# Kernel tuning notes

Measured on AMD Instinct MI355X. Metric: run time of the kernel, lower is better.

The kernel has to match this reference:

```python
import jax, jax.numpy as jnp
import numpy as np

NUM_CLASSES = 512  # P distinct identities in the batch (labels are in [0, P))
TAU = 0.5
EPS = 1e-12


def _l2norm(x):
    # F.normalize(x, dim=1) with eps clamp
    n = jnp.sqrt(jnp.sum(x * x, axis=1, keepdims=True))
    return x / jnp.maximum(n, EPS)


def setup_inputs() -> dict:
    key = jax.random.key(0)
    k1, k2, k3 = jax.random.split(key, 3)
    N, D, P = 8192, 2048, NUM_CLASSES
    feat_vp = jax.random.normal(k1, (N, D), dtype=jnp.float32)
    feat_ap = jax.random.normal(k2, (N, D), dtype=jnp.float32)
    feat_rp = jax.random.normal(k3, (N, D), dtype=jnp.float32)
    # P identities, K = N/P instances each; every class present
    label = (jnp.arange(N) % P).astype(jnp.int32)
    return {"feat_vp": feat_vp, "feat_ap": feat_ap, "feat_rp": feat_rp, "label": label}


def reference(feat_vp, feat_ap, feat_rp, label):
    P = NUM_CLASSES
    fv = _l2norm(feat_vp)
    fa = _l2norm(feat_ap)
    fr = _l2norm(feat_rp)

    # segment-mean over labels (replaces the O(N^2 D) python loop)
    counts = jax.ops.segment_sum(jnp.ones_like(label, dtype=fv.dtype), label,
                                 num_segments=P)  # [P]
    inv_cnt = 1.0 / counts[:, None]

    def centers(f):
        s = jax.ops.segment_sum(f, label, num_segments=P)  # [P, D]
        return _l2norm(s * inv_cnt)

    cv, ca, cr = centers(fv), centers(fa), centers(fr)

    # per-sample centers = unique centers gathered back by label
    loss_intra = (jnp.sum((fv - cv[label]) ** 2, axis=1).mean()
                  + jnp.sum((fa - ca[label]) ** 2, axis=1).mean()
                  + jnp.sum((fr - cr[label]) ** 2, axis=1).mean())

    def pair_loss(c1, c2):
        logits = (c1 @ c2.T) / TAU  # [P, P]
        logp = jax.nn.log_softmax(logits, axis=1)
        return -jnp.mean(jnp.diagonal(logp))

    loss_inter = pair_loss(cv, ca) + pair_loss(cv, cr) + pair_loss(ca, cr)
    return loss_intra + loss_inter
```

## Files before the change

### kernel.cpp

```cpp
#include <hip/hip_runtime.h>
#include <hip/hip_bf16.h>

#define P_CLS 512
#define D_DIM 2048
#define CAP   32
#define TAU_INV 2.0f

typedef short short8 __attribute__((ext_vector_type(8)));
typedef float f32x4 __attribute__((ext_vector_type(4)));

__device__ __forceinline__ unsigned short f2bf_bits(float x) {
  __hip_bfloat16 b = __float2bfloat16(x);
  unsigned short u;
  __builtin_memcpy(&u, &b, sizeof(u));
  return u;
}

__device__ __forceinline__ float xred_sum(float v) {
#pragma unroll
  for (int o = 1; o < 64; o <<= 1) v += __shfl_xor(v, o, 64);
  return v;
}
__device__ __forceinline__ float xred_max(float v) {
#pragma unroll
  for (int o = 1; o < 64; o <<= 1) v = fmaxf(v, __shfl_xor(v, o, 64));
  return v;
}

__global__ void k_init(int* cnt, float* accs) {
  int t = blockIdx.x * blockDim.x + threadIdx.x;
  if (t < P_CLS) cnt[t] = 0;
  if (t < 8) accs[t] = 0.f;
}

__global__ void k_index(const int* __restrict__ label, int* __restrict__ cnt,
                        int* __restrict__ idx, int n) {
  int i = blockIdx.x * blockDim.x + threadIdx.x;
  if (i < n) {
    int p = label[i];
    int slot = atomicAdd(&cnt[p], 1);
    if (slot < CAP) idx[p * CAP + slot] = i;
  }
}

__global__ __launch_bounds__(256)
void k_centers(const float* __restrict__ f0, const float* __restrict__ f1,
               const float* __restrict__ f2, const int* __restrict__ cnt,
               const int* __restrict__ idx, __hip_bfloat16* __restrict__ cb,
               float* __restrict__ accs) {
  __shared__ __align__(16) f32x4 red[4][D_DIM / 4];
  __shared__ float scr[4];
  int p = blockIdx.x, m = blockIdx.y;
  const float* F = (m == 0) ? f0 : (m == 1) ? f1 : f2;
  int t = threadIdx.x, lane = t & 63, wv = t >> 6;
  int c = cnt[p];
  if (c > CAP) c = CAP;
  const int* idxp = idx + p * CAP;

  int nr = (c > wv) ? ((c - wv + 3) >> 2) : 0;

  f32x4 acc[8] = {{0,0,0,0},{0,0,0,0},{0,0,0,0},{0,0,0,0},
                  {0,0,0,0},{0,0,0,0},{0,0,0,0},{0,0,0,0}};
  f32x4 a[8], b[8];

  auto loadrow = [&](f32x4* buf, int r) {
    const f32x4* rp = (const f32x4*)(F + (long)idxp[r] * D_DIM);
#pragma unroll
    for (int j = 0; j < 8; ++j) buf[j] = rp[lane + 64 * j];
  };
  auto consume = [&](const f32x4* buf) {
    float ssq = 0.f;
#pragma unroll
    for (int j = 0; j < 8; ++j) {
      f32x4 q = buf[j] * buf[j];
      ssq += q.x + q.y + q.z + q.w;
    }
    ssq = xred_sum(ssq);
    float w = 1.0f / fmaxf(sqrtf(ssq), 1e-12f);
#pragma unroll
    for (int j = 0; j < 8; ++j) acc[j] += buf[j] * w;
  };

  if (nr > 0) loadrow(a, wv);
  if (nr > 1) loadrow(b, wv + 4);
  for (int k = 0; k < nr; k += 2) {
    consume(a);
    if (k + 2 < nr) loadrow(a, wv + 4 * (k + 2));
    if (k + 1 < nr) {
      consume(b);
      if (k + 3 < nr) loadrow(b, wv + 4 * (k + 3));
    }
  }

#pragma unroll
  for (int j = 0; j < 8; ++j) red[wv][lane + 64 * j] = acc[j];
  __syncthreads();
  f32x4 s0 = red[0][t] + red[1][t] + red[2][t] + red[3][t];
  f32x4 s1 = red[0][t + 256] + red[1][t + 256] + red[2][t + 256] + red[3][t + 256];
  f32x4 q0 = s0 * s0, q1 = s1 * s1;
  float s2 = q0.x + q0.y + q0.z + q0.w + q1.x + q1.y + q1.z + q1.w;
  s2 = xred_sum(s2);
  if (lane == 0) scr[wv] = s2;
  __syncthreads();
  s2 = scr[0] + scr[1] + scr[2] + scr[3];
  float sn = sqrtf(s2);
  float inv = 1.0f / fmaxf(sn, 1e-12f);
  __hip_bfloat16* dst = cb + ((long)m * P_CLS + p) * D_DIM;
  f32x4 o0 = s0 * inv, o1 = s1 * inv;
  ushort4 h0, h1;
  h0.x = f2bf_bits(o0.x); h0.y = f2bf_bits(o0.y);
  h0.z = f2bf_bits(o0.z); h0.w = f2bf_bits(o0.w);
  h1.x = f2bf_bits(o1.x); h1.y = f2bf_bits(o1.y);
  h1.z = f2bf_bits(o1.z); h1.w = f2bf_bits(o1.w);
  ((ushort4*)dst)[t] = h0;
  ((ushort4*)dst)[t + 256] = h1;
  if (t == 0 && c > 0) atomicAdd(&accs[0], sn);
}

__global__ __launch_bounds__(256)
void k_gemm(const __hip_bfloat16* __restrict__ cbh, float* __restrict__ logits) {
  __shared__ __align__(16) unsigned short As[2][64 * 40], Bs[2][64 * 40];
  int pair = blockIdx.y, kz = blockIdx.z, nkz = gridDim.z;
  int ksl = D_DIM / nkz;
  int ma = (pair == 2) ? 1 : 0;
  int mb = (pair == 0) ? 1 : 2;
  const unsigned short* A =
      (const unsigned short*)cbh + (long)ma * P_CLS * D_DIM + kz * ksl;
  const unsigned short* B =
      (const unsigned short*)cbh + (long)mb * P_CLS * D_DIM + kz * ksl;
  float* C = logits + ((long)kz * 3 + pair) * P_CLS * P_CLS;
  int tm = (blockIdx.x >> 3) * 64, tn = (blockIdx.x & 7) * 64;
  int t = threadIdx.x, lane = t & 63, wv = t >> 6;
  int srow = t >> 2, skc = (t & 3) * 8;
  int quad = lane >> 4, mr = lane & 15;
  const unsigned short* pa = A + (long)(tm + srow) * D_DIM + skc;
  const unsigned short* pb = B + (long)(tn + srow) * D_DIM + skc;
  f32x4 acc[4] = {{0,0,0,0},{0,0,0,0},{0,0,0,0},{0,0,0,0}};
  uint4 av = *(const uint4*)pa, bv = *(const uint4*)pb;
  *(uint4*)(&As[0][srow * 40 + skc]) = av;
  *(uint4*)(&Bs[0][srow * 40 + skc]) = bv;
  av = *(const uint4*)(pa + 32); bv = *(const uint4*)(pb + 32);
  const int NIT = ksl / 32;
  for (int it = 0; it < NIT; ++it) {
    __syncthreads();
    int cur = it & 1;
    if (it + 1 < NIT) {
      *(uint4*)(&As[cur ^ 1][srow * 40 + skc]) = av;
      *(uint4*)(&Bs[cur ^ 1][srow * 40 + skc]) = bv;
    }
    if (it + 2 < NIT) {
      av = *(const uint4*)(pa + (it + 2) * 32);
      bv = *(const uint4*)(pb + (it + 2) * 32);
    }
    short8 af = *(const short8*)(&As[cur][(wv * 16 + mr) * 40 + quad * 8]);
#pragma unroll
    for (int nb = 0; nb < 4; ++nb) {
      short8 bfr = *(const short8*)(&Bs[cur][(nb * 16 + mr) * 40 + quad * 8]);
      acc[nb] = __builtin_amdgcn_mfma_f32_16x16x32_bf16(af, bfr, acc[nb], 0, 0, 0);
    }
  }
  int crow = tm + wv * 16 + quad * 4;
#pragma unroll
  for (int nb = 0; nb < 4; ++nb)
#pragma unroll
    for (int r = 0; r < 4; ++r)
      C[(long)(crow + r) * P_CLS + tn + nb * 16 + mr] = acc[nb][r] * TAU_INV;
}

__global__ __launch_bounds__(256)
void k_lse(const float* __restrict__ logits, float* __restrict__ accs, int nkz) {
  __shared__ float sred[8];
  int row = blockIdx.x;
  int p = row & (P_CLS - 1);
  int t = threadIdx.x, lane = t & 63, wv = t >> 6;
  float v0 = 0.f, v1 = 0.f, diag = 0.f;
  for (int z = 0; z < nkz; ++z) {
    const float* L = logits + ((long)z * 3 * P_CLS + row) * P_CLS;
    v0 += L[t];
    v1 += L[t + 256];
  }
  float mx = xred_max(fmaxf(v0, v1));
  if (lane == 0) sred[wv] = mx;
  __syncthreads();
  mx = fmaxf(fmaxf(sred[0], sred[1]), fmaxf(sred[2], sred[3]));
  float e = expf(v0 - mx) + expf(v1 - mx);
  e = xred_sum(e);
  if (lane == 0) sred[4 + wv] = e;
  __syncthreads();
  if (t == 0) {
    float tot = sred[4] + sred[5] + sred[6] + sred[7];
    for (int z = 0; z < nkz; ++z)
      diag += logits[((long)z * 3 * P_CLS + row) * P_CLS + p];
    atomicAdd(&accs[1], mx + logf(tot) - diag);
  }
}

__global__ void k_final(const float* __restrict__ accs, float* __restrict__ out,
                        float invN) {
  out[0] = 6.0f - 2.0f * invN * accs[0] + accs[1] * (1.0f / (float)P_CLS);
}

extern "C" void kernel_launch(void* const* d_in, const int* in_sizes, int n_in,
                              void* d_out, int out_size, void* d_ws, size_t ws_size,
                              hipStream_t stream) {
  const float* fvp = (const float*)d_in[0];
  const float* fap = (const float*)d_in[1];
  const float* frp = (const float*)d_in[2];
  const int* label = (const int*)d_in[3];
  int N = in_sizes[3];

  char* ws = (char*)d_ws;
  int* cnt = (int*)ws;
  int* idx = (int*)(ws + 2048);
  float* accs = (float*)(ws + 2048 + 65536);
  __hip_bfloat16* cb = (__hip_bfloat16*)(ws + 131072);
  float* logits = (float*)(ws + 131072 + 3ul * P_CLS * D_DIM * 2);

  size_t base = 131072 + 3ul * P_CLS * D_DIM * 2;
  size_t per_z = 3ul * P_CLS * P_CLS * 4;
  int KZ = (ws_size >= base + 4 * per_z) ? 4 : 2;

  hipLaunchKernelGGL(k_init, dim3(1), dim3(512), 0, stream, cnt, accs);
  hipLaunchKernelGGL(k_index, dim3((N + 255) / 256), dim3(256), 0, stream,
                     label, cnt, idx, N);
  hipLaunchKernelGGL(k_centers, dim3(P_CLS, 3), dim3(256), 0, stream,
                     fvp, fap, frp, cnt, idx, cb, accs);
  hipLaunchKernelGGL(k_gemm, dim3(64, 3, KZ), dim3(256), 0, stream, cb, logits);
  hipLaunchKernelGGL(k_lse, dim3(3 * P_CLS), dim3(256), 0, stream, logits, accs, KZ);
  hipLaunchKernelGGL(k_final, dim3(1), dim3(1), 0, stream, accs, (float*)d_out,
                     1.0f / (float)N);
}
```

Measured before the change: 238.7 us.

## Widen center blocks to 16 waves with LDS atomics; fold final into LSE

The centers kernel now launches 1024 threads per class, so each wave loads at most two rows at once instead of pipelining eight rows across four waves. Per-wave partial sums are combined through LDS float atomics into a padded (bank-skewed) shared buffer, and a single wave then normalizes and writes the center. The separate final kernel is dropped: the last LSE block, found with an atomic done counter, computes the output. This raises memory-level parallelism and removes one launch, at the cost of LDS atomic contention, a single-wave epilogue, and fewer co-resident blocks.

```diff
diff --git a/kernel.cpp b/kernel.cpp
--- a/kernel.cpp
+++ b/kernel.cpp
@@ -5,6 +5,8 @@
 #define D_DIM 2048
 #define CAP   32
 #define TAU_INV 2.0f
+
+#define SW(a) ((a) + ((a) >> 5))
 
 typedef short short8 __attribute__((ext_vector_type(8)));
 typedef float f32x4 __attribute__((ext_vector_type(4)));
@@ -27,10 +29,11 @@
   return v;
 }
 
-__global__ void k_init(int* cnt, float* accs) {
+__global__ void k_init(int* cnt, float* accs, int* done) {
   int t = blockIdx.x * blockDim.x + threadIdx.x;
   if (t < P_CLS) cnt[t] = 0;
   if (t < 8) accs[t] = 0.f;
+  if (t == 8) *done = 0;
 }
 
 __global__ void k_index(const int* __restrict__ label, int* __restrict__ cnt,
@@ -43,13 +46,12 @@
   }
 }
 
-__global__ __launch_bounds__(256)
+__global__ __launch_bounds__(1024)
 void k_centers(const float* __restrict__ f0, const float* __restrict__ f1,
                const float* __restrict__ f2, const int* __restrict__ cnt,
                const int* __restrict__ idx, __hip_bfloat16* __restrict__ cb,
                float* __restrict__ accs) {
-  __shared__ __align__(16) f32x4 red[4][D_DIM / 4];
-  __shared__ float scr[4];
+  __shared__ float scen[D_DIM + D_DIM / 32];
   int p = blockIdx.x, m = blockIdx.y;
   const float* F = (m == 0) ? f0 : (m == 1) ? f1 : f2;
   int t = threadIdx.x, lane = t & 63, wv = t >> 6;
@@ -57,64 +59,67 @@
   if (c > CAP) c = CAP;
   const int* idxp = idx + p * CAP;
 
-  int nr = (c > wv) ? ((c - wv + 3) >> 2) : 0;
-
-  f32x4 acc[8] = {{0,0,0,0},{0,0,0,0},{0,0,0,0},{0,0,0,0},
-                  {0,0,0,0},{0,0,0,0},{0,0,0,0},{0,0,0,0}};
-  f32x4 a[8], b[8];
-
-  auto loadrow = [&](f32x4* buf, int r) {
-    const f32x4* rp = (const f32x4*)(F + (long)idxp[r] * D_DIM);
-#pragma unroll
-    for (int j = 0; j < 8; ++j) buf[j] = rp[lane + 64 * j];
-  };
-  auto consume = [&](const f32x4* buf) {
-    float ssq = 0.f;
+  scen[t] = 0.f;
+  scen[t + 1024] = 0.f;
+  if (t < D_DIM / 32) scen[t + 2048] = 0.f;
+  __syncthreads();
+
+#pragma unroll
+  for (int s = 0; s < 2; ++s) {
+    int r = wv + 16 * s;
+    if (r < c) {
+      const f32x4* rp = (const f32x4*)(F + (long)idxp[r] * D_DIM) + lane;
+      f32x4 buf[8];
+#pragma unroll
+      for (int j = 0; j < 8; ++j) buf[j] = rp[64 * j];
+      float ssq = 0.f;
+#pragma unroll
+      for (int j = 0; j < 8; ++j) {
+        f32x4 q = buf[j] * buf[j];
+        ssq += q.x + q.y + q.z + q.w;
+      }
+      ssq = xred_sum(ssq);
+      float w = 1.0f / fmaxf(sqrtf(ssq), 1e-12f);
+#pragma unroll
+      for (int j = 0; j < 8; ++j) {
+        f32x4 v = buf[j] * w;
+        int e = SW(4 * lane + 256 * j);
+        atomicAdd(&scen[e + 0], v.x);
+        atomicAdd(&scen[e + 1], v.y);
+        atomicAdd(&scen[e + 2], v.z);
+        atomicAdd(&scen[e + 3], v.w);
+      }
+    }
+  }
+  __syncthreads();
+
+  if (wv == 0) {
+    f32x4 sv[8];
+    float s2 = 0.f;
 #pragma unroll
     for (int j = 0; j < 8; ++j) {
-      f32x4 q = buf[j] * buf[j];
-      ssq += q.x + q.y + q.z + q.w;
-    }
-    ssq = xred_sum(ssq);
-    float w = 1.0f / fmaxf(sqrtf(ssq), 1e-12f);
-#pragma unroll
-    for (int j = 0; j < 8; ++j) acc[j] += buf[j] * w;
-  };
-
-  if (nr > 0) loadrow(a, wv);
-  if (nr > 1) loadrow(b, wv + 4);
-  for (int k = 0; k < nr; k += 2) {
-    consume(a);
-    if (k + 2 < nr) loadrow(a, wv + 4 * (k + 2));
-    if (k + 1 < nr) {
-      consume(b);
-      if (k + 3 < nr) loadrow(b, wv + 4 * (k + 3));
-    }
-  }
-
-#pragma unroll
-  for (int j = 0; j < 8; ++j) red[wv][lane + 64 * j] = acc[j];
-  __syncthreads();
-  f32x4 s0 = red[0][t] + red[1][t] + red[2][t] + red[3][t];
-  f32x4 s1 = red[0][t + 256] + red[1][t + 256] + red[2][t + 256] + red[3][t + 256];
-  f32x4 q0 = s0 * s0, q1 = s1 * s1;
-  float s2 = q0.x + q0.y + q0.z + q0.w + q1.x + q1.y + q1.z + q1.w;
-  s2 = xred_sum(s2);
-  if (lane == 0) scr[wv] = s2;
-  __syncthreads();
-  s2 = scr[0] + scr[1] + scr[2] + scr[3];
-  float sn = sqrtf(s2);
-  float inv = 1.0f / fmaxf(sn, 1e-12f);
-  __hip_bfloat16* dst = cb + ((long)m * P_CLS + p) * D_DIM;
-  f32x4 o0 = s0 * inv, o1 = s1 * inv;
-  ushort4 h0, h1;
-  h0.x = f2bf_bits(o0.x); h0.y = f2bf_bits(o0.y);
-  h0.z = f2bf_bits(o0.z); h0.w = f2bf_bits(o0.w);
-  h1.x = f2bf_bits(o1.x); h1.y = f2bf_bits(o1.y);
-  h1.z = f2bf_bits(o1.z); h1.w = f2bf_bits(o1.w);
-  ((ushort4*)dst)[t] = h0;
-  ((ushort4*)dst)[t + 256] = h1;
-  if (t == 0 && c > 0) atomicAdd(&accs[0], sn);
+      int e = SW(4 * lane + 256 * j);
+      sv[j].x = scen[e + 0];
+      sv[j].y = scen[e + 1];
+      sv[j].z = scen[e + 2];
+      sv[j].w = scen[e + 3];
+      f32x4 q = sv[j] * sv[j];
+      s2 += q.x + q.y + q.z + q.w;
+    }
+    s2 = xred_sum(s2);
+    float sn = sqrtf(s2);
+    float inv = 1.0f / fmaxf(sn, 1e-12f);
+    __hip_bfloat16* dst = cb + ((long)m * P_CLS + p) * D_DIM;
+#pragma unroll
+    for (int j = 0; j < 8; ++j) {
+      f32x4 o = sv[j] * inv;
+      ushort4 h;
+      h.x = f2bf_bits(o.x); h.y = f2bf_bits(o.y);
+      h.z = f2bf_bits(o.z); h.w = f2bf_bits(o.w);
+      ((ushort4*)dst)[lane + 64 * j] = h;
+    }
+    if (lane == 0 && c > 0) atomicAdd(&accs[0], sn);
+  }
 }
 
 __global__ __launch_bounds__(256)
@@ -168,7 +173,8 @@
 }
 
 __global__ __launch_bounds__(256)
-void k_lse(const float* __restrict__ logits, float* __restrict__ accs, int nkz) {
+void k_lse(const float* __restrict__ logits, float* __restrict__ accs, int nkz,
+           int* __restrict__ done, float* __restrict__ out, float invN) {
   __shared__ float sred[8];
   int row = blockIdx.x;
   int p = row & (P_CLS - 1);
@@ -192,12 +198,14 @@
     for (int z = 0; z < nkz; ++z)
       diag += logits[((long)z * 3 * P_CLS + row) * P_CLS + p];
     atomicAdd(&accs[1], mx + logf(tot) - diag);
-  }
-}
-
-__global__ void k_final(const float* __restrict__ accs, float* __restrict__ out,
-                        float invN) {
-  out[0] = 6.0f - 2.0f * invN * accs[0] + accs[1] * (1.0f / (float)P_CLS);
+    __threadfence();
+    int prev = atomicAdd(done, 1);
+    if (prev == 3 * P_CLS - 1) {
+      float a0 = atomicAdd(&accs[0], 0.f);
+      float a1 = atomicAdd(&accs[1], 0.f);
+      out[0] = 6.0f - 2.0f * invN * a0 + a1 * (1.0f / (float)P_CLS);
+    }
+  }
 }
 
 extern "C" void kernel_launch(void* const* d_in, const int* in_sizes, int n_in,
@@ -213,6 +221,7 @@
   int* cnt = (int*)ws;
   int* idx = (int*)(ws + 2048);
   float* accs = (float*)(ws + 2048 + 65536);
+  int* done = (int*)(ws + 2048 + 65536 + 32);
   __hip_bfloat16* cb = (__hip_bfloat16*)(ws + 131072);
   float* logits = (float*)(ws + 131072 + 3ul * P_CLS * D_DIM * 2);
 
@@ -220,13 +229,12 @@
   size_t per_z = 3ul * P_CLS * P_CLS * 4;
   int KZ = (ws_size >= base + 4 * per_z) ? 4 : 2;
 
-  hipLaunchKernelGGL(k_init, dim3(1), dim3(512), 0, stream, cnt, accs);
+  hipLaunchKernelGGL(k_init, dim3(1), dim3(512), 0, stream, cnt, accs, done);
   hipLaunchKernelGGL(k_index, dim3((N + 255) / 256), dim3(256), 0, stream,
                      label, cnt, idx, N);
-  hipLaunchKernelGGL(k_centers, dim3(P_CLS, 3), dim3(256), 0, stream,
+  hipLaunchKernelGGL(k_centers, dim3(P_CLS, 3), dim3(1024), 0, stream,
                      fvp, fap, frp, cnt, idx, cb, accs);
   hipLaunchKernelGGL(k_gemm, dim3(64, 3, KZ), dim3(256), 0, stream, cb, logits);
-  hipLaunchKernelGGL(k_lse, dim3(3 * P_CLS), dim3(256), 0, stream, logits, accs, KZ);
-  hipLaunchKernelGGL(k_final, dim3(1), dim3(1), 0, stream, accs, (float*)d_out,
-                     1.0f / (float)N);
-}
+  hipLaunchKernelGGL(k_lse, dim3(3 * P_CLS), dim3(256), 0, stream, logits, accs,
+                     KZ, done, (float*)d_out, 1.0f / (float)N);
+}
```

New measurement: 457.0 us. 1.91x slower.

## Precompute per-row inverse norms in a separate pass before center accumulation

Applied to the files above, without the earlier changes.

Adds a kernel that computes the inverse L2 norm of every feature row and stores it in workspace. The centers kernel then uses the whole block to accumulate 16 weighted rows at a time, which gives more independent loads in flight and removes the cross-wave LDS reduction. The aim is to cut the latency-bound serial norm, then accumulate chain in the centers kernel. In exchange every feature matrix is read from memory twice, unless the second read hits cache, and an extra launch is added.

```diff
diff --git a/kernel.cpp b/kernel.cpp
--- a/kernel.cpp
+++ b/kernel.cpp
@@ -44,11 +44,33 @@
 }
 
 __global__ __launch_bounds__(256)
+void k_norms(const float* __restrict__ f0, const float* __restrict__ f1,
+             const float* __restrict__ f2, float* __restrict__ wnorm, int n) {
+  int m = blockIdx.y;
+  const float* F = (m == 0) ? f0 : (m == 1) ? f1 : f2;
+  int t = threadIdx.x, lane = t & 63, wv = t >> 6;
+  int row = blockIdx.x * 4 + wv;
+  if (row >= n) return;
+  const f32x4* rp = (const f32x4*)(F + (long)row * D_DIM) + lane;
+  f32x4 b[8];
+#pragma unroll
+  for (int j = 0; j < 8; ++j) b[j] = rp[64 * j];
+  float ssq = 0.f;
+#pragma unroll
+  for (int j = 0; j < 8; ++j) {
+    f32x4 q = b[j] * b[j];
+    ssq += q.x + q.y + q.z + q.w;
+  }
+  ssq = xred_sum(ssq);
+  if (lane == 0) wnorm[(long)m * n + row] = 1.0f / fmaxf(sqrtf(ssq), 1e-12f);
+}
+
+__global__ __launch_bounds__(256)
 void k_centers(const float* __restrict__ f0, const float* __restrict__ f1,
                const float* __restrict__ f2, const int* __restrict__ cnt,
-               const int* __restrict__ idx, __hip_bfloat16* __restrict__ cb,
-               float* __restrict__ accs) {
-  __shared__ __align__(16) f32x4 red[4][D_DIM / 4];
+               const int* __restrict__ idx, const float* __restrict__ wnorm,
+               __hip_bfloat16* __restrict__ cb, float* __restrict__ accs,
+               int n) {
   __shared__ float scr[4];
   int p = blockIdx.x, m = blockIdx.y;
   const float* F = (m == 0) ? f0 : (m == 1) ? f1 : f2;
@@ -56,49 +78,28 @@
   int c = cnt[p];
   if (c > CAP) c = CAP;
   const int* idxp = idx + p * CAP;
-
-  int nr = (c > wv) ? ((c - wv + 3) >> 2) : 0;
-
-  f32x4 acc[8] = {{0,0,0,0},{0,0,0,0},{0,0,0,0},{0,0,0,0},
-                  {0,0,0,0},{0,0,0,0},{0,0,0,0},{0,0,0,0}};
-  f32x4 a[8], b[8];
-
-  auto loadrow = [&](f32x4* buf, int r) {
-    const f32x4* rp = (const f32x4*)(F + (long)idxp[r] * D_DIM);
-#pragma unroll
-    for (int j = 0; j < 8; ++j) buf[j] = rp[lane + 64 * j];
-  };
-  auto consume = [&](const f32x4* buf) {
-    float ssq = 0.f;
-#pragma unroll
-    for (int j = 0; j < 8; ++j) {
-      f32x4 q = buf[j] * buf[j];
-      ssq += q.x + q.y + q.z + q.w;
-    }
-    ssq = xred_sum(ssq);
-    float w = 1.0f / fmaxf(sqrtf(ssq), 1e-12f);
-#pragma unroll
-    for (int j = 0; j < 8; ++j) acc[j] += buf[j] * w;
-  };
-
-  if (nr > 0) loadrow(a, wv);
-  if (nr > 1) loadrow(b, wv + 4);
-  for (int k = 0; k < nr; k += 2) {
-    consume(a);
-    if (k + 2 < nr) loadrow(a, wv + 4 * (k + 2));
-    if (k + 1 < nr) {
-      consume(b);
-      if (k + 3 < nr) loadrow(b, wv + 4 * (k + 3));
-    }
-  }
-
-#pragma unroll
-  for (int j = 0; j < 8; ++j) red[wv][lane + 64 * j] = acc[j];
-  __syncthreads();
-  f32x4 s0 = red[0][t] + red[1][t] + red[2][t] + red[3][t];
-  f32x4 s1 = red[0][t + 256] + red[1][t + 256] + red[2][t + 256] + red[3][t + 256];
-  f32x4 q0 = s0 * s0, q1 = s1 * s1;
-  float s2 = q0.x + q0.y + q0.z + q0.w + q1.x + q1.y + q1.z + q1.w;
+  const float* wn = wnorm + (long)m * n;
+
+  f32x4 acc0 = {0, 0, 0, 0}, acc1 = {0, 0, 0, 0};
+  for (int base = 0; base < c; base += 16) {
+    const int4* ip4 = (const int4*)(idxp + base);
+    int4 iv0 = ip4[0], iv1 = ip4[1], iv2 = ip4[2], iv3 = ip4[3];
+    int rr[16] = {iv0.x, iv0.y, iv0.z, iv0.w, iv1.x, iv1.y, iv1.z, iv1.w,
+                  iv2.x, iv2.y, iv2.z, iv2.w, iv3.x, iv3.y, iv3.z, iv3.w};
+#pragma unroll
+    for (int r = 0; r < 16; ++r) {
+      if (base + r < c) {
+        int ri = rr[r];
+        float wr = wn[ri];
+        const f32x4* rp = (const f32x4*)(F + (long)ri * D_DIM);
+        acc0 += rp[t] * wr;
+        acc1 += rp[t + 256] * wr;
+      }
+    }
+  }
+
+  f32x4 qa = acc0 * acc0, qb = acc1 * acc1;
+  float s2 = qa.x + qa.y + qa.z + qa.w + qb.x + qb.y + qb.z + qb.w;
   s2 = xred_sum(s2);
   if (lane == 0) scr[wv] = s2;
   __syncthreads();
@@ -106,7 +107,7 @@
   float sn = sqrtf(s2);
   float inv = 1.0f / fmaxf(sn, 1e-12f);
   __hip_bfloat16* dst = cb + ((long)m * P_CLS + p) * D_DIM;
-  f32x4 o0 = s0 * inv, o1 = s1 * inv;
+  f32x4 o0 = acc0 * inv, o1 = acc1 * inv;
   ushort4 h0, h1;
   h0.x = f2bf_bits(o0.x); h0.y = f2bf_bits(o0.y);
   h0.z = f2bf_bits(o0.z); h0.w = f2bf_bits(o0.w);
@@ -213,18 +214,21 @@
   int* cnt = (int*)ws;
   int* idx = (int*)(ws + 2048);
   float* accs = (float*)(ws + 2048 + 65536);
-  __hip_bfloat16* cb = (__hip_bfloat16*)(ws + 131072);
-  float* logits = (float*)(ws + 131072 + 3ul * P_CLS * D_DIM * 2);
-
-  size_t base = 131072 + 3ul * P_CLS * D_DIM * 2;
+  float* wnorm = (float*)(ws + 69632);
+  __hip_bfloat16* cb = (__hip_bfloat16*)(ws + 262144);
+  float* logits = (float*)(ws + 262144 + 3ul * P_CLS * D_DIM * 2);
+
+  size_t base = 262144 + 3ul * P_CLS * D_DIM * 2;
   size_t per_z = 3ul * P_CLS * P_CLS * 4;
   int KZ = (ws_size >= base + 4 * per_z) ? 4 : 2;
 
   hipLaunchKernelGGL(k_init, dim3(1), dim3(512), 0, stream, cnt, accs);
   hipLaunchKernelGGL(k_index, dim3((N + 255) / 256), dim3(256), 0, stream,
                      label, cnt, idx, N);
+  hipLaunchKernelGGL(k_norms, dim3((N + 3) / 4, 3), dim3(256), 0, stream,
+                     fvp, fap, frp, wnorm, N);
   hipLaunchKernelGGL(k_centers, dim3(P_CLS, 3), dim3(256), 0, stream,
-                     fvp, fap, frp, cnt, idx, cb, accs);
+                     fvp, fap, frp, cnt, idx, wnorm, cb, accs, N);
   hipLaunchKernelGGL(k_gemm, dim3(64, 3, KZ), dim3(256), 0, stream, cb, logits);
   hipLaunchKernelGGL(k_lse, dim3(3 * P_CLS), dim3(256), 0, stream, logits, accs, KZ);
   hipLaunchKernelGGL(k_final, dim3(1), dim3(1), 0, stream, accs, (float*)d_out,
```

After: 276.9 us. +16.0%, slower.
